# Kernel tuning notes

Measured on AMD Instinct MI355X. Metric: run time of the kernel, lower is better.

The kernel has to match this reference:

```python
import jax, jax.numpy as jnp
import numpy as np

EPS = 1e-5
GROUPS = 8


def setup_inputs() -> dict:
    key = jax.random.key(0)
    ks = jax.random.split(key, 7)
    B, C, L = 16, 512, 4096
    x = jax.random.normal(ks[0], (B, C, L), dtype=jnp.float32)
    gamma = jnp.ones((C,), jnp.float32)
    beta = jnp.zeros((C,), jnp.float32)
    # Conv1d kernel_size=1 weights -> plain matrices
    w1 = jax.random.normal(ks[1], (2 * C, C), jnp.float32) / np.sqrt(C)
    b1 = jax.random.normal(ks[2], (2 * C,), jnp.float32) * 0.01
    w2 = jax.random.normal(ks[3], (C, 2 * C), jnp.float32) / np.sqrt(2 * C)
    b2 = jax.random.normal(ks[4], (C,), jnp.float32) * 0.01
    return {"x": x, "gamma": gamma, "beta": beta, "w1": w1, "b1": b1, "w2": w2, "b2": b2}


def _group_norm(x, gamma, beta):
    B, C, L = x.shape
    xg = x.reshape(B, GROUPS, C // GROUPS, L)
    mean = jnp.mean(xg, axis=(2, 3), keepdims=True)
    var = jnp.var(xg, axis=(2, 3), keepdims=True)
    xn = ((xg - mean) * jax.lax.rsqrt(var + EPS)).reshape(B, C, L)
    return xn * gamma[None, :, None] + beta[None, :, None]


def reference(x, gamma, beta, w1, b1, w2, b2):
    h = _group_norm(x, gamma, beta)                      # [B, C, L]
    h = jnp.einsum('bcl,dc->bdl', h, w1) + b1[None, :, None]  # [B, 2C, L]
    h = jax.nn.gelu(h, approximate=False)
    h = jnp.einsum('bdl,cd->bcl', h, w2) + b2[None, :, None]  # [B, C, L]
    return x + h
```

## Files before the change

### kernel.cpp

```cpp
#include <hip/hip_runtime.h>
#include <cstdint>
#include <cstddef>


typedef unsigned short u16;
typedef unsigned int u32;
typedef __attribute__((ext_vector_type(8))) __bf16 bf16x8;
typedef __attribute__((ext_vector_type(4))) float floatx4;

#define BM 128
#define BN 128
#define BKK 64

__device__ __forceinline__ u16 f2bf(float f) {
    union { float f; u32 u; } v; v.f = f;
    u32 u = v.u;
    return (u16)((u + 0x7fffu + ((u >> 16) & 1u)) >> 16);
}

__device__ __forceinline__ float gelu_exact(float v) {
    const float x = fabsf(v) * 0.70710678118654752f;
    const float t = __builtin_amdgcn_rcpf(fmaf(0.3275911f, x, 1.0f));
    float p = fmaf(1.061405429f, t, -1.453152027f);
    p = fmaf(p, t, 1.421413741f);
    p = fmaf(p, t, -0.284496736f);
    p = fmaf(p, t, 0.254829592f);
    p = p * t;
    const float e = __expf(-x * x);
    const float er = fmaf(-p, e, 1.0f);
    const float s = copysignf(er, v);
    return 0.5f * v * (1.0f + s);
}

__device__ __forceinline__ void async_cp16(u16* lds, const u16* g) {
    __builtin_amdgcn_global_load_lds(
        (const __attribute__((address_space(1))) u32*)g,
        (__attribute__((address_space(3))) u32*)lds,
        16, 0, 0);
}

__global__ __launch_bounds__(256) void gn_stats_partial(const float* __restrict__ x,
                                                        float* __restrict__ pstats) {
    const int bx = blockIdx.x;
    const float4* p = (const float4*)(x + (size_t)(bx >> 3) * 262144 + (size_t)(bx & 7) * 32768);
    float s = 0.f, ss = 0.f;
    for (int i = threadIdx.x; i < 8192; i += 256) {
        float4 v = p[i];
        s += v.x + v.y + v.z + v.w;
        ss += v.x * v.x + v.y * v.y + v.z * v.z + v.w * v.w;
    }
#pragma unroll
    for (int off = 32; off > 0; off >>= 1) {
        s  += __shfl_down(s, off, 64);
        ss += __shfl_down(ss, off, 64);
    }
    __shared__ float rs[8];
    const int wv = threadIdx.x >> 6;
    if ((threadIdx.x & 63) == 0) { rs[wv * 2] = s; rs[wv * 2 + 1] = ss; }
    __syncthreads();
    if (threadIdx.x == 0) {
        pstats[bx * 2]     = rs[0] + rs[2] + rs[4] + rs[6];
        pstats[bx * 2 + 1] = rs[1] + rs[3] + rs[5] + rs[7];
    }
}

__global__ __launch_bounds__(256) void conv_w(const float* __restrict__ w1,
                                              const float* __restrict__ w2,
                                              u16* __restrict__ wb) {
    const int idx = (blockIdx.x * 256 + threadIdx.x) * 4;
    const float4 v = (idx < 524288) ? *(const float4*)(w1 + idx)
                                    : *(const float4*)(w2 + (idx - 524288));
    ushort4 o;
    o.x = f2bf(v.x); o.y = f2bf(v.y); o.z = f2bf(v.z); o.w = f2bf(v.w);
    *(ushort4*)(wb + idx) = o;
}

__global__ __launch_bounds__(256) void gn_norm_tr(const float* __restrict__ x,
                                                  const float* __restrict__ gamma,
                                                  const float* __restrict__ beta,
                                                  const float* __restrict__ pstats,
                                                  u16* __restrict__ xnT, int b0) {
    __shared__ u16 T[64][72];
    const int bx = blockIdx.x;
    const int lt = bx & 63, ct = (bx >> 6) & 7, bl = bx >> 9;
    const int b = b0 + bl;
    const int c0 = ct * 64, l0 = lt * 64;
    const int g = c0 >> 6;
    float S = 0.f, SS = 0.f;
#pragma unroll
    for (int s2 = 0; s2 < 8; ++s2) {
        S  += pstats[((b * 8 + g) * 8 + s2) * 2];
        SS += pstats[((b * 8 + g) * 8 + s2) * 2 + 1];
    }
    const float inv = 1.f / 262144.f;
    const float mean = S * inv;
    const float var = SS * inv - mean * mean;
    const float rstd = rsqrtf(var + 1e-5f);

    const int t = threadIdx.x;
    const int cl = t >> 3;
    const int lo = (t & 7) * 8;
    const int sw = t & 7;
#pragma unroll
    for (int h = 0; h < 2; ++h) {
        const int c = c0 + cl + h * 32;
        const float sc = rstd * gamma[c];
        const float sh = beta[c] - mean * sc;
        const float* src = x + ((size_t)(b * 512 + c) * 4096 + l0 + lo);
        float4 a = *(const float4*)src;
        float4 bq = *(const float4*)(src + 4);
        float vv[8] = {a.x, a.y, a.z, a.w, bq.x, bq.y, bq.z, bq.w};
        const int ccol = cl + h * 32;
        const int cg = ccol >> 3, cr = ccol & 7;
#pragma unroll
        for (int q = 0; q < 8; ++q)
            T[lo + q][((cg ^ sw) << 3) + cr] = f2bf(fmaf(vv[q], sc, sh));
    }
    __syncthreads();
    const int ll = t >> 3;
    const int co = (t & 7) * 8, cog = t & 7;
#pragma unroll
    for (int h = 0; h < 2; ++h) {
        const int l = ll + h * 32;
        const uint4* srcv = (const uint4*)&T[l][(cog ^ ((l >> 3) & 7)) << 3];
        *(uint4*)(xnT + ((size_t)(bl * 4096 + l0 + l) * 512 + c0 + co)) = *srcv;
    }
}

__device__ __forceinline__ void gemm_core(const u16* __restrict__ Ag,
                                          const u16* __restrict__ Bg,
                                          int K, floatx4 acc[4][4],
                                          u16* lA, u16* lB,
                                          int wm, int wn, int fr, int quad) {
    const int t = threadIdx.x;
    for (int kt = 0; kt < K; kt += BKK) {
#pragma unroll
        for (int s = 0; s < 4; ++s) {
            int idx = s * 256 + t;
            int row = idx >> 3;
            int kg = (idx & 7) ^ (row & 7);
            async_cp16(lA + idx * 8, Ag + (size_t)row * K + kt + kg * 8);
        }
#pragma unroll
        for (int s = 0; s < 4; ++s) {
            int idx = s * 256 + t;
            int row = idx >> 3;
            int kg = (idx & 7) ^ (row & 7);
            async_cp16(lB + idx * 8, Bg + (size_t)row * K + kt + kg * 8);
        }
        __syncthreads();
#pragma unroll
        for (int kk = 0; kk < BKK; kk += 32) {
            bf16x8 af[4], bb[4];
#pragma unroll
            for (int i = 0; i < 4; ++i) {
                int row = wm + i * 16 + fr;
                int kg = ((kk >> 3) + quad) ^ (fr & 7);
                af[i] = *(const bf16x8*)(lA + row * BKK + kg * 8);
            }
#pragma unroll
            for (int j = 0; j < 4; ++j) {
                int row = wn + j * 16 + fr;
                int kg = ((kk >> 3) + quad) ^ (fr & 7);
                bb[j] = *(const bf16x8*)(lB + row * BKK + kg * 8);
            }
#pragma unroll
            for (int i = 0; i < 4; ++i)
#pragma unroll
                for (int j = 0; j < 4; ++j)
                    acc[i][j] = __builtin_amdgcn_mfma_f32_16x16x32_bf16(bb[j], af[i], acc[i][j], 0, 0, 0);
        }
        __syncthreads();
    }
}

__global__ __launch_bounds__(256) void gemm1(const u16* __restrict__ xnT,
                                             const u16* __restrict__ w1b,
                                             const float* __restrict__ b1,
                                             u16* __restrict__ h1T) {
    __shared__ uint4 lAq[BM * BKK / 8], lBq[BN * BKK / 8];
    u16* lA = (u16*)lAq; u16* lB = (u16*)lBq;
    const int bx = blockIdx.x;
    const int nt = (bx >> 3) & 7;
    const int mt = (bx & 7) | ((bx >> 6) << 3);
    const int t = threadIdx.x, lane = t & 63, wv = t >> 6;
    const int wm = (wv & 1) * 64, wn = (wv >> 1) * 64;
    const int fr = lane & 15, quad = lane >> 4;
    floatx4 acc[4][4];
#pragma unroll
    for (int i = 0; i < 4; ++i)
#pragma unroll
        for (int j = 0; j < 4; ++j) acc[i][j] = (floatx4){0.f, 0.f, 0.f, 0.f};

    gemm_core(xnT + (size_t)(mt * BM) * 512, w1b + (size_t)(nt * BN) * 512, 512,
              acc, lA, lB, wm, wn, fr, quad);

    const int mb = mt * BM + wm + fr;
    const int nb = nt * BN + wn + quad * 4;
#pragma unroll
    for (int j = 0; j < 4; ++j) {
        const int n0 = nb + j * 16;
        const float4 bv = *(const float4*)(b1 + n0);
#pragma unroll
        for (int i = 0; i < 4; ++i) {
            const int m = mb + i * 16;
            ushort4 o;
            o.x = f2bf(gelu_exact(acc[i][j][0] + bv.x));
            o.y = f2bf(gelu_exact(acc[i][j][1] + bv.y));
            o.z = f2bf(gelu_exact(acc[i][j][2] + bv.z));
            o.w = f2bf(gelu_exact(acc[i][j][3] + bv.w));
            *(ushort4*)(h1T + (size_t)m * 1024 + n0) = o;
        }
    }
}

__global__ __launch_bounds__(256) void gemm2(const u16* __restrict__ w2b,
                                             const u16* __restrict__ h1T,
                                             const float* __restrict__ b2,
                                             const float* __restrict__ x,
                                             float* __restrict__ out, int b0) {
    __shared__ uint4 lAq[BM * BKK / 8], lBq[BN * BKK / 8];
    u16* lA = (u16*)lAq; u16* lB = (u16*)lBq;
    const int bx = blockIdx.x;
    const int mt = (bx >> 3) & 3;
    const int nt = (bx & 7) | ((bx >> 5) << 3);
    const int t = threadIdx.x, lane = t & 63, wv = t >> 6;
    const int wm = (wv & 1) * 64, wn = (wv >> 1) * 64;
    const int fr = lane & 15, quad = lane >> 4;
    floatx4 acc[4][4];
#pragma unroll
    for (int i = 0; i < 4; ++i)
#pragma unroll
        for (int j = 0; j < 4; ++j) acc[i][j] = (floatx4){0.f, 0.f, 0.f, 0.f};

    gemm_core(w2b + (size_t)(mt * BM) * 1024, h1T + (size_t)(nt * BN) * 1024, 1024,
              acc, lA, lB, wm, wn, fr, quad);

    const int n0g = b0 * 4096 + nt * BN;
    const int b = n0g >> 12;
    const int l_base = n0g & 4095;
    const int mb = mt * BM + wm + fr;
    const int nb = wn + quad * 4;
#pragma unroll
    for (int i = 0; i < 4; ++i) {
        const int m = mb + i * 16;
        const float bv = b2[m];
        const size_t rowoff = ((size_t)(b * 512 + m)) * 4096 + l_base + nb;
#pragma unroll
        for (int j = 0; j < 4; ++j) {
            const float4 xv = *(const float4*)(x + rowoff + j * 16);
            float4 ov;
            ov.x = acc[i][j][0] + bv + xv.x;
            ov.y = acc[i][j][1] + bv + xv.y;
            ov.z = acc[i][j][2] + bv + xv.z;
            ov.w = acc[i][j][3] + bv + xv.w;
            *(float4*)(out + rowoff + j * 16) = ov;
        }
    }
}

extern "C" void kernel_launch(void* const* d_in, const int* in_sizes, int n_in,
                              void* d_out, int out_size, void* d_ws, size_t ws_size,
                              hipStream_t stream) {
    const float* x     = (const float*)d_in[0];
    const float* gamma = (const float*)d_in[1];
    const float* beta  = (const float*)d_in[2];
    const float* w1    = (const float*)d_in[3];
    const float* b1    = (const float*)d_in[4];
    const float* w2    = (const float*)d_in[5];
    const float* b2    = (const float*)d_in[6];
    float* out = (float*)d_out;

    char* ws = (char*)d_ws;
    float* pstats = (float*)ws;
    u16* wb = (u16*)(ws + 65536);
    char* chunkbase = ws + 65536 + (2u << 20);
    const size_t fixed = 65536 + (2u << 20);

    const size_t per = (size_t)192 * 1024 * 1024;
    int NC = 16;
    if      (ws_size >= fixed + per)      NC = 1;
    else if (ws_size >= fixed + per / 2)  NC = 2;
    else if (ws_size >= fixed + per / 4)  NC = 4;
    else if (ws_size >= fixed + per / 8)  NC = 8;
    const int CB = 16 / NC;
    u16* xnT = (u16*)chunkbase;
    u16* h1T = (u16*)(chunkbase + (size_t)CB * 4096 * 512 * 2);

    gn_stats_partial<<<1024, 256, 0, stream>>>(x, pstats);
    conv_w<<<1024, 256, 0, stream>>>(w1, w2, wb);
    for (int ch = 0; ch < NC; ++ch) {
        const int b0 = ch * CB;
        gn_norm_tr<<<CB * 512, 256, 0, stream>>>(x, gamma, beta, pstats, xnT, b0);
        gemm1<<<CB * 32 * 8, 256, 0, stream>>>(xnT, wb, b1, h1T);
        gemm2<<<CB * 32 * 4, 256, 0, stream>>>(wb + 524288, h1T, b2, x, out, b0);
    }
}
```

Baseline: 506.7 us.

## Use 256x256 tiles with 8 waves and double-buffered async LDS pipeline in GEMMs

Replaces the 128x128 single-buffered GEMM core with a 256x256 tile computed by 512 threads (8 waves). Global-to-LDS copies are split into half-K stages that are double-buffered and prefetched two phases ahead, with explicit vmcnt waits, barriers and setprio around the MFMA bursts. Tile-to-workgroup mapping is remapped for XCD locality. The aim is to overlap loads with MFMA and raise arithmetic intensity, at the cost of 128KB of LDS per block, more registers, and fewer workgroups per launch, which can leave CUs underused when chunks are small.

```diff
diff --git a/kernel.cpp b/kernel.cpp
--- a/kernel.cpp
+++ b/kernel.cpp
@@ -8,8 +8,6 @@
 typedef __attribute__((ext_vector_type(8))) __bf16 bf16x8;
 typedef __attribute__((ext_vector_type(4))) float floatx4;
 
-#define BM 128
-#define BN 128
 #define BKK 64
 
 __device__ __forceinline__ u16 f2bf(float f) {
@@ -127,82 +125,110 @@
     }
 }
 
-__device__ __forceinline__ void gemm_core(const u16* __restrict__ Ag,
-                                          const u16* __restrict__ Bg,
-                                          int K, floatx4 acc[4][4],
-                                          u16* lA, u16* lB,
-                                          int wm, int wn, int fr, int quad) {
-    const int t = threadIdx.x;
-    for (int kt = 0; kt < K; kt += BKK) {
-#pragma unroll
-        for (int s = 0; s < 4; ++s) {
-            int idx = s * 256 + t;
-            int row = idx >> 3;
-            int kg = (idx & 7) ^ (row & 7);
-            async_cp16(lA + idx * 8, Ag + (size_t)row * K + kt + kg * 8);
-        }
-#pragma unroll
-        for (int s = 0; s < 4; ++s) {
-            int idx = s * 256 + t;
-            int row = idx >> 3;
-            int kg = (idx & 7) ^ (row & 7);
-            async_cp16(lB + idx * 8, Bg + (size_t)row * K + kt + kg * 8);
-        }
-        __syncthreads();
-#pragma unroll
-        for (int kk = 0; kk < BKK; kk += 32) {
-            bf16x8 af[4], bb[4];
-#pragma unroll
-            for (int i = 0; i < 4; ++i) {
-                int row = wm + i * 16 + fr;
-                int kg = ((kk >> 3) + quad) ^ (fr & 7);
-                af[i] = *(const bf16x8*)(lA + row * BKK + kg * 8);
-            }
-#pragma unroll
-            for (int j = 0; j < 4; ++j) {
-                int row = wn + j * 16 + fr;
-                int kg = ((kk >> 3) + quad) ^ (fr & 7);
-                bb[j] = *(const bf16x8*)(lB + row * BKK + kg * 8);
-            }
-#pragma unroll
-            for (int i = 0; i < 4; ++i)
-#pragma unroll
-                for (int j = 0; j < 4; ++j)
-                    acc[i][j] = __builtin_amdgcn_mfma_f32_16x16x32_bf16(bb[j], af[i], acc[i][j], 0, 0, 0);
-        }
-        __syncthreads();
-    }
-}
-
-__global__ __launch_bounds__(256) void gemm1(const u16* __restrict__ xnT,
-                                             const u16* __restrict__ w1b,
-                                             const float* __restrict__ b1,
-                                             u16* __restrict__ h1T) {
-    __shared__ uint4 lAq[BM * BKK / 8], lBq[BN * BKK / 8];
-    u16* lA = (u16*)lAq; u16* lB = (u16*)lBq;
+__device__ __forceinline__ void stage_half(u16* ldsOp, const u16* gOp, int K,
+                                           int tile, int kh, int tid) {
+    u16* dst = ldsOp + ((tile & 1) * 16384 + kh * 8192);
+    const u16* src = gOp + (size_t)tile * BKK + kh * 32;
+#pragma unroll
+    for (int s = 0; s < 2; ++s) {
+        int idx2 = s * 512 + tid;
+        int row = idx2 >> 2;
+        int g2 = (idx2 & 3) ^ ((row >> 1) & 3);
+        async_cp16(dst + idx2 * 8, src + (size_t)row * K + g2 * 8);
+    }
+}
+
+#define VM8 { asm volatile("s_waitcnt vmcnt(8)" ::: "memory"); \
+              __builtin_amdgcn_sched_barrier(0); }
+
+__device__ __forceinline__ void gemm_core256(const u16* __restrict__ Ag,
+                                             const u16* __restrict__ Bg,
+                                             int K, int NT, floatx4 acc[8][4],
+                                             u16* lA, u16* lB,
+                                             int wm, int wn, int fr, int quad) {
+    const int tid = threadIdx.x;
+    const int sl4 = quad ^ ((fr >> 1) & 3);
+    bf16x8 bb[4];
+
+    stage_half(lA, Ag, K, 0, 0, tid); stage_half(lB, Bg, K, 0, 0, tid);
+    stage_half(lA, Ag, K, 0, 1, tid); stage_half(lB, Bg, K, 0, 1, tid);
+    stage_half(lA, Ag, K, 1, 0, tid); stage_half(lB, Bg, K, 1, 0, tid);
+    asm volatile("s_waitcnt vmcnt(8)" ::: "memory");
+    __builtin_amdgcn_sched_barrier(0);
+    __builtin_amdgcn_s_barrier();
+
+#define PHASE(kh_, ih_, STG, DOVM)                                              \
+    {                                                                           \
+        const u16* bA = lA + ((t & 1) * 16384 + (kh_) * 8192);                  \
+        const u16* bB = lB + ((t & 1) * 16384 + (kh_) * 8192);                  \
+        bf16x8 af[4];                                                           \
+        _Pragma("unroll")                                                       \
+        for (int i = 0; i < 4; ++i)                                             \
+            af[i] = *(const bf16x8*)(bA + ((((wm + (ih_)*64 + i*16 + fr) << 2) | sl4) * 8)); \
+        if ((ih_) == 0) {                                                       \
+            _Pragma("unroll")                                                   \
+            for (int j = 0; j < 4; ++j)                                         \
+                bb[j] = *(const bf16x8*)(bB + ((((wn + j*16 + fr) << 2) | sl4) * 8)); \
+        }                                                                       \
+        STG;                                                                    \
+        __builtin_amdgcn_s_barrier();                                           \
+        __builtin_amdgcn_s_setprio(1);                                          \
+        _Pragma("unroll")                                                       \
+        for (int j = 0; j < 4; ++j) {                                           \
+            _Pragma("unroll")                                                   \
+            for (int i = 0; i < 4; ++i)                                         \
+                acc[(ih_)*4 + i][j] = __builtin_amdgcn_mfma_f32_16x16x32_bf16(  \
+                    bb[j], af[i], acc[(ih_)*4 + i][j], 0, 0, 0);                \
+        }                                                                       \
+        __builtin_amdgcn_s_setprio(0);                                          \
+        DOVM;                                                                   \
+        __builtin_amdgcn_s_barrier();                                           \
+    }
+
+    for (int t = 0; t < NT; ++t) {
+        int t1 = t + 1; if (t1 >= NT) t1 -= NT;
+        int t2 = t + 2; if (t2 >= NT) t2 -= NT;
+        PHASE(0, 0, stage_half(lA, Ag, K, t1, 1, tid), {})
+        PHASE(0, 1, stage_half(lB, Bg, K, t1, 1, tid), VM8)
+        PHASE(1, 0, stage_half(lA, Ag, K, t2, 0, tid), {})
+        PHASE(1, 1, stage_half(lB, Bg, K, t2, 0, tid), VM8)
+    }
+#undef PHASE
+    asm volatile("s_waitcnt vmcnt(0)" ::: "memory");
+    __builtin_amdgcn_sched_barrier(0);
+}
+
+__global__ __launch_bounds__(512, 2) void gemm1(const u16* __restrict__ xnT,
+                                                const u16* __restrict__ w1b,
+                                                const float* __restrict__ b1,
+                                                u16* __restrict__ h1T) {
+    __shared__ u16 lds[65536];
+    u16* lA = lds;
+    u16* lB = lds + 32768;
     const int bx = blockIdx.x;
-    const int nt = (bx >> 3) & 7;
-    const int mt = (bx & 7) | ((bx >> 6) << 3);
-    const int t = threadIdx.x, lane = t & 63, wv = t >> 6;
-    const int wm = (wv & 1) * 64, wn = (wv >> 1) * 64;
+    const int xcd = bx & 7;
+    const int nt = (bx >> 3) & 3;
+    const int mt = (bx >> 5) * 8 + xcd;
+    const int tid = threadIdx.x, lane = tid & 63, wid = tid >> 6;
+    const int wm = (wid >> 2) * 128, wn = (wid & 3) * 64;
     const int fr = lane & 15, quad = lane >> 4;
-    floatx4 acc[4][4];
-#pragma unroll
-    for (int i = 0; i < 4; ++i)
+    floatx4 acc[8][4];
+#pragma unroll
+    for (int i = 0; i < 8; ++i)
 #pragma unroll
         for (int j = 0; j < 4; ++j) acc[i][j] = (floatx4){0.f, 0.f, 0.f, 0.f};
 
-    gemm_core(xnT + (size_t)(mt * BM) * 512, w1b + (size_t)(nt * BN) * 512, 512,
-              acc, lA, lB, wm, wn, fr, quad);
-
-    const int mb = mt * BM + wm + fr;
-    const int nb = nt * BN + wn + quad * 4;
+    gemm_core256(xnT + (size_t)(mt * 256) * 512, w1b + (size_t)(nt * 256) * 512,
+                 512, 8, acc, lA, lB, wm, wn, fr, quad);
+
+    const int mb = mt * 256 + wm + fr;
+    const int nb = nt * 256 + wn + quad * 4;
 #pragma unroll
     for (int j = 0; j < 4; ++j) {
         const int n0 = nb + j * 16;
         const float4 bv = *(const float4*)(b1 + n0);
 #pragma unroll
-        for (int i = 0; i < 4; ++i) {
+        for (int i = 0; i < 8; ++i) {
             const int m = mb + i * 16;
             ushort4 o;
             o.x = f2bf(gelu_exact(acc[i][j][0] + bv.x));
@@ -214,35 +240,37 @@
     }
 }
 
-__global__ __launch_bounds__(256) void gemm2(const u16* __restrict__ w2b,
-                                             const u16* __restrict__ h1T,
-                                             const float* __restrict__ b2,
-                                             const float* __restrict__ x,
-                                             float* __restrict__ out, int b0) {
-    __shared__ uint4 lAq[BM * BKK / 8], lBq[BN * BKK / 8];
-    u16* lA = (u16*)lAq; u16* lB = (u16*)lBq;
+__global__ __launch_bounds__(512, 2) void gemm2(const u16* __restrict__ w2b,
+                                                const u16* __restrict__ h1T,
+                                                const float* __restrict__ b2,
+                                                const float* __restrict__ x,
+                                                float* __restrict__ out, int b0) {
+    __shared__ u16 lds[65536];
+    u16* lA = lds;
+    u16* lB = lds + 32768;
     const int bx = blockIdx.x;
-    const int mt = (bx >> 3) & 3;
-    const int nt = (bx & 7) | ((bx >> 5) << 3);
-    const int t = threadIdx.x, lane = t & 63, wv = t >> 6;
-    const int wm = (wv & 1) * 64, wn = (wv >> 1) * 64;
+    const int xcd = bx & 7;
+    const int mt = (bx >> 3) & 1;
+    const int nt = (bx >> 4) * 8 + xcd;
+    const int tid = threadIdx.x, lane = tid & 63, wid = tid >> 6;
+    const int wm = (wid >> 2) * 128, wn = (wid & 3) * 64;
     const int fr = lane & 15, quad = lane >> 4;
-    floatx4 acc[4][4];
-#pragma unroll
-    for (int i = 0; i < 4; ++i)
+    floatx4 acc[8][4];
+#pragma unroll
+    for (int i = 0; i < 8; ++i)
 #pragma unroll
         for (int j = 0; j < 4; ++j) acc[i][j] = (floatx4){0.f, 0.f, 0.f, 0.f};
 
-    gemm_core(w2b + (size_t)(mt * BM) * 1024, h1T + (size_t)(nt * BN) * 1024, 1024,
-              acc, lA, lB, wm, wn, fr, quad);
-
-    const int n0g = b0 * 4096 + nt * BN;
+    gemm_core256(w2b + (size_t)(mt * 256) * 1024, h1T + (size_t)(nt * 256) * 1024,
+                 1024, 16, acc, lA, lB, wm, wn, fr, quad);
+
+    const int n0g = b0 * 4096 + nt * 256;
     const int b = n0g >> 12;
     const int l_base = n0g & 4095;
-    const int mb = mt * BM + wm + fr;
+    const int mb = mt * 256 + wm + fr;
     const int nb = wn + quad * 4;
 #pragma unroll
-    for (int i = 0; i < 4; ++i) {
+    for (int i = 0; i < 8; ++i) {
         const int m = mb + i * 16;
         const float bv = b2[m];
         const size_t rowoff = ((size_t)(b * 512 + m)) * 4096 + l_base + nb;
@@ -292,7 +320,7 @@
     for (int ch = 0; ch < NC; ++ch) {
         const int b0 = ch * CB;
         gn_norm_tr<<<CB * 512, 256, 0, stream>>>(x, gamma, beta, pstats, xnT, b0);
-        gemm1<<<CB * 32 * 8, 256, 0, stream>>>(xnT, wb, b1, h1T);
-        gemm2<<<CB * 32 * 4, 256, 0, stream>>>(wb + 524288, h1T, b2, x, out, b0);
-    }
-}
+        gemm1<<<CB * 64, 512, 0, stream>>>(xnT, wb, b1, h1T);
+        gemm2<<<CB * 32, 512, 0, stream>>>(wb + 524288, h1T, b2, x, out, b0);
+    }
+}
```

Result: faster. 486.4 us (-4.0%).
